# Optimization experiments

Measured on AMD Instinct MI355X. Metric: run time of the kernel, lower is better.

## Reference

```python
import jax, jax.numpy as jnp
import numpy as np

K = 8          # filter_volume = 2^3
N_IN = 1600000 # active input sites
R = 200000     # rules per filter offset (each input site used once total)
N_OUT = 400000 # active output sites
C_IN = 32
C_OUT = 32


def setup_inputs() -> dict:
    key = jax.random.key(0)
    k1, k2, k3, k4 = jax.random.split(key, 4)
    std = (2.0 * 1 / C_IN / K) ** 0.5  # SCN init: sqrt(2*groups/nIn/filter_volume)
    input_features = jax.random.normal(k1, (N_IN, C_IN), dtype=jnp.float32)
    weight = jax.random.normal(k2, (K, 1, C_IN, C_OUT), dtype=jnp.float32) * std
    bias = jnp.zeros((C_OUT,), dtype=jnp.float32)
    # Rulebook: per filter offset f, pairs (rules_in[f,r] -> rules_out[f,r]).
    # For a 2^3/stride-2 conv each input site appears exactly once overall;
    # a random permutation split into K chunks models that structure.
    perm = jax.random.permutation(k3, N_IN)[: K * R]
    rules_in = perm.reshape(K, R).astype(jnp.int32)
    rules_out = jax.random.randint(k4, (K, R), 0, N_OUT, dtype=jnp.int32)
    return {
        "input_features": input_features,
        "weight": weight,
        "bias": bias,
        "rules_in": rules_in,
        "rules_out": rules_out,
        "n_out": N_OUT,
    }


def reference(input_features, weight, bias, rules_in, rules_out, n_out):
    # gather -> per-offset GEMM -> scatter-add (groups == 1)
    gathered = input_features[rules_in]                 # [K, R, C_in]
    w = weight[:, 0]                                    # [K, C_in, C_out]
    contrib = jnp.einsum("krc,kco->kro", gathered, w)   # [K, R, C_out]
    out = jnp.zeros((n_out, contrib.shape[-1]), dtype=input_features.dtype)
    out = out.at[rules_out.reshape(-1)].add(contrib.reshape(-1, contrib.shape[-1]))
    return out + bias
```

## Files before the change

### kernel.cpp

```cpp
#include <hip/hip_runtime.h>
#include <stdint.h>

#define KTAPS 8
#define C 32
#define CAPR 16
#define OMAX 8192

__global__ __launch_bounds__(256) void init_kernel(
    unsigned int* __restrict__ counts, int n_cnt4) {
  int i = blockIdx.x * 256 + threadIdx.x;
  if (i < n_cnt4) ((uint4*)counts)[i] = make_uint4(0u, 0u, 0u, 0u);
}

__global__ __launch_bounds__(256) void contrib_kernel(
    const float* __restrict__ in, const float* __restrict__ w,
    const int* __restrict__ rules_in, const int* __restrict__ rules_out,
    unsigned int* __restrict__ counts, unsigned int* __restrict__ bidx,
    uint2* __restrict__ oflow, unsigned int* __restrict__ ocount,
    float* __restrict__ contrib, int R) {
  const int k = blockIdx.y;
  const int r = blockIdx.x * 256 + threadIdx.x;
  if (r >= R) return;

  const int ri = rules_in[k * R + r];
  const int ro = rules_out[k * R + r];

  const float4* rowp = (const float4*)(in + (size_t)ri * C);
  float4 av[8];
#pragma unroll
  for (int j = 0; j < 8; ++j) av[j] = rowp[j];

  const unsigned int slot = atomicAdd(counts + (unsigned int)ro, 1u);

  float a[C];
#pragma unroll
  for (int j = 0; j < 8; ++j) {
    a[4 * j + 0] = av[j].x; a[4 * j + 1] = av[j].y;
    a[4 * j + 2] = av[j].z; a[4 * j + 3] = av[j].w;
  }

  const float* wk = w + k * (C * C);
  float acc[C];
#pragma unroll
  for (int co = 0; co < C; ++co) acc[co] = a[0] * wk[co];
#pragma unroll
  for (int ci = 1; ci < C; ++ci)
#pragma unroll
    for (int co = 0; co < C; ++co)
      acc[co] = fmaf(a[ci], wk[ci * C + co], acc[co]);

  const unsigned int t = (unsigned int)(k * R + r);
  float4* cp = (float4*)(contrib + (size_t)t * C);
#pragma unroll
  for (int j = 0; j < 8; ++j)
    cp[j] = make_float4(acc[4 * j + 0], acc[4 * j + 1],
                        acc[4 * j + 2], acc[4 * j + 3]);

  if (slot < (unsigned int)CAPR) {
    bidx[(size_t)(unsigned int)ro * CAPR + slot] = t;
  } else {
    unsigned int j = atomicAdd(ocount, 1u);
    if (j < (unsigned int)OMAX) oflow[j] = make_uint2((unsigned int)ro, t);
  }
}

__global__ __launch_bounds__(256) void reduce_kernel(
    const unsigned int* __restrict__ counts,
    const unsigned int* __restrict__ bidx,
    const float* __restrict__ contrib, const float* __restrict__ bias,
    float* __restrict__ out, int n_out) {
  const int g    = threadIdx.x >> 5;
  const int lane = threadIdx.x & 31;
  const int rowA = (blockIdx.x * 8 + g) * 2;
  if (rowA >= n_out) return;
  const int rowB = rowA + 1;

  const unsigned int bval = bidx[(size_t)rowA * CAPR + lane];
  unsigned int cntA = counts[rowA]; if (cntA > (unsigned int)CAPR) cntA = CAPR;
  unsigned int cntB = counts[rowB]; if (cntB > (unsigned int)CAPR) cntB = CAPR;

  float vA[CAPR], vB[CAPR];
#pragma unroll
  for (int j = 0; j < CAPR; ++j) {
    const unsigned int tA = (unsigned int)__shfl((int)bval, j, 32);
    const unsigned int sA = (j < (int)cntA) ? tA : 0u;
    vA[j] = contrib[(size_t)sA * C + lane];
  }
#pragma unroll
  for (int j = 0; j < CAPR; ++j) {
    const unsigned int tB = (unsigned int)__shfl((int)bval, CAPR + j, 32);
    const unsigned int sB = (j < (int)cntB) ? tB : 0u;
    vB[j] = contrib[(size_t)sB * C + lane];
  }

  const float b = bias[lane];
  float accA = b, accB = b;
#pragma unroll
  for (int j = 0; j < CAPR; ++j) {
    accA += (j < (int)cntA) ? vA[j] : 0.f;
    accB += (j < (int)cntB) ? vB[j] : 0.f;
  }

  out[(size_t)rowA * C + lane] = accA;
  out[(size_t)rowB * C + lane] = accB;
}

__global__ __launch_bounds__(256) void oflow_kernel(
    const uint2* __restrict__ oflow, const unsigned int* __restrict__ ocount,
    const float* __restrict__ contrib, float* __restrict__ out) {
  const int g  = threadIdx.x >> 5;
  const int co = threadIdx.x & 31;
  unsigned int n = *ocount;
  if (n > (unsigned int)OMAX) n = (unsigned int)OMAX;
  for (unsigned int e = blockIdx.x * 8 + g; e < n; e += gridDim.x * 8) {
    const uint2 ent = oflow[e];
    unsafeAtomicAdd(out + (size_t)ent.x * C + co,
                    contrib[(size_t)ent.y * C + co]);
  }
}

__global__ __launch_bounds__(256) void bias_init_kernel(
    float* __restrict__ out, const float* __restrict__ bias, int n4) {
  int idx = blockIdx.x * 256 + threadIdx.x;
  if (idx >= n4) return;
  ((float4*)out)[idx] = ((const float4*)bias)[idx & 7];
}

__global__ __launch_bounds__(256) void scatter_gemm_kernel(
    const float* __restrict__ in, const float* __restrict__ w,
    const int* __restrict__ rules_in, const int* __restrict__ rules_out,
    float* __restrict__ out, int R) {
  const int k = blockIdx.y;
  const int r = blockIdx.x * 256 + threadIdx.x;
  if (r >= R) return;
  const int ri = rules_in[k * R + r];
  const int ro = rules_out[k * R + r];
  const float4* rowp = (const float4*)(in + (size_t)ri * C);
  float a[C];
#pragma unroll
  for (int j = 0; j < 8; ++j) {
    float4 vv = rowp[j];
    a[4 * j + 0] = vv.x; a[4 * j + 1] = vv.y;
    a[4 * j + 2] = vv.z; a[4 * j + 3] = vv.w;
  }
  const float* wk = w + k * (C * C);
  float acc[C];
#pragma unroll
  for (int co = 0; co < C; ++co) acc[co] = a[0] * wk[co];
#pragma unroll
  for (int ci = 1; ci < C; ++ci)
#pragma unroll
    for (int co = 0; co < C; ++co)
      acc[co] = fmaf(a[ci], wk[ci * C + co], acc[co]);
  float* op = out + (size_t)ro * C;
#pragma unroll
  for (int co = 0; co < C; ++co) unsafeAtomicAdd(op + co, acc[co]);
}

extern "C" void kernel_launch(void* const* d_in, const int* in_sizes, int n_in,
                              void* d_out, int out_size, void* d_ws, size_t ws_size,
                              hipStream_t stream) {
  const float* in_features = (const float*)d_in[0];
  const float* weight      = (const float*)d_in[1];
  const float* bias        = (const float*)d_in[2];
  const int*   rules_in    = (const int*)d_in[3];
  const int*   rules_out   = (const int*)d_in[4];

  const int R     = in_sizes[3] / KTAPS;
  const int n_out = out_size / C;
  float* out = (float*)d_out;

  const size_t n_cnt     = ((size_t)n_out + 16) & ~(size_t)3;
  const size_t counts_b  = n_cnt * sizeof(unsigned int);
  const size_t bidx_b    = (size_t)n_out * CAPR * sizeof(unsigned int);
  const size_t oflow_b   = (size_t)OMAX * sizeof(uint2);
  const size_t n_rules   = (size_t)KTAPS * R;
  const size_t contrib_b = n_rules * C * sizeof(float);

  if (ws_size >= counts_b + bidx_b + oflow_b + contrib_b) {
    unsigned int* counts  = (unsigned int*)d_ws;
    unsigned int* ocount  = counts + n_out;
    unsigned int* bidx    = (unsigned int*)((char*)d_ws + counts_b);
    uint2*        oflow   = (uint2*)((char*)d_ws + counts_b + bidx_b);
    float*        contrib = (float*)((char*)d_ws + counts_b + bidx_b + oflow_b);

    const int n_cnt4 = (int)(n_cnt / 4);
    init_kernel<<<(n_cnt4 + 255) / 256, 256, 0, stream>>>(counts, n_cnt4);

    dim3 gridB((R + 255) / 256, KTAPS);
    contrib_kernel<<<gridB, 256, 0, stream>>>(in_features, weight, rules_in,
                                              rules_out, counts, bidx, oflow,
                                              ocount, contrib, R);

    const int rows_per_block = 16;
    reduce_kernel<<<(n_out + rows_per_block - 1) / rows_per_block, 256, 0,
                    stream>>>(counts, bidx, contrib, bias, out, n_out);

    oflow_kernel<<<32, 256, 0, stream>>>(oflow, ocount, contrib, out);
  } else {
    const int n_out4 = out_size / 4;
    bias_init_kernel<<<(n_out4 + 255) / 256, 256, 0, stream>>>(out, bias, n_out4);
    dim3 grid((R + 255) / 256, KTAPS);
    scatter_gemm_kernel<<<grid, 256, 0, stream>>>(in_features, weight, rules_in,
                                                  rules_out, out, R);
  }
}
```

Measured before the change: 471.3 us.

## Fuse GEMM and scatter with LDS-transposed coalesced atomics, drop bucketed reduction

Replaces the contribution-buffer plus bucketed-reduction pipeline with a single kernel that computes each rule's 32-wide GEMM row, stages it in padded shared memory, and issues row-coalesced float atomics directly into the bias-initialised output. This removes the large intermediate contrib write/read and the count/index bookkeeping. In exchange it relies on atomic throughput to random output rows and gives up deterministic summation order.

```diff
diff --git a/kernel.cpp b/kernel.cpp
--- a/kernel.cpp
+++ b/kernel.cpp
@@ -3,34 +3,40 @@
 
 #define KTAPS 8
 #define C 32
-#define CAPR 16
-#define OMAX 8192
+#define LDSS 33
 
-__global__ __launch_bounds__(256) void init_kernel(
-    unsigned int* __restrict__ counts, int n_cnt4) {
-  int i = blockIdx.x * 256 + threadIdx.x;
-  if (i < n_cnt4) ((uint4*)counts)[i] = make_uint4(0u, 0u, 0u, 0u);
+__global__ __launch_bounds__(256) void bias_init_kernel(
+    float* __restrict__ out, const float* __restrict__ bias, int n4) {
+  int idx = blockIdx.x * 256 + threadIdx.x;
+  if (idx >= n4) return;
+  ((float4*)out)[idx] = ((const float4*)bias)[idx & 7];
 }
 
-__global__ __launch_bounds__(256) void contrib_kernel(
+__global__ __launch_bounds__(256) void fused_scatter_kernel(
     const float* __restrict__ in, const float* __restrict__ w,
     const int* __restrict__ rules_in, const int* __restrict__ rules_out,
-    unsigned int* __restrict__ counts, unsigned int* __restrict__ bidx,
-    uint2* __restrict__ oflow, unsigned int* __restrict__ ocount,
-    float* __restrict__ contrib, int R) {
-  const int k = blockIdx.y;
-  const int r = blockIdx.x * 256 + threadIdx.x;
-  if (r >= R) return;
+    float* __restrict__ out, int R) {
+  __shared__ float cbuf[256 * LDSS];
+  __shared__ int   robuf[256];
 
-  const int ri = rules_in[k * R + r];
-  const int ro = rules_out[k * R + r];
+  const int k     = blockIdx.y;
+  const int tid   = threadIdx.x;
+  const int r     = blockIdx.x * 256 + tid;
+  const int lane  = tid & 63;
+  const int wbase = tid & ~63;
+
+  if (blockIdx.x * 256 + wbase >= R) return;
+
+  const bool valid = (r < R);
+  const int rc = valid ? r : (R - 1);
+  const int ri = rules_in[(size_t)k * R + rc];
+  const int ro = valid ? rules_out[(size_t)k * R + rc] : -1;
+  robuf[tid] = ro;
 
   const float4* rowp = (const float4*)(in + (size_t)ri * C);
   float4 av[8];
 #pragma unroll
   for (int j = 0; j < 8; ++j) av[j] = rowp[j];
-
-  const unsigned int slot = atomicAdd(counts + (unsigned int)ro, 1u);
 
   float a[C];
 #pragma unroll
@@ -49,112 +55,20 @@
     for (int co = 0; co < C; ++co)
       acc[co] = fmaf(a[ci], wk[ci * C + co], acc[co]);
 
-  const unsigned int t = (unsigned int)(k * R + r);
-  float4* cp = (float4*)(contrib + (size_t)t * C);
+  float* myrow = cbuf + tid * LDSS;
 #pragma unroll
-  for (int j = 0; j < 8; ++j)
-    cp[j] = make_float4(acc[4 * j + 0], acc[4 * j + 1],
-                        acc[4 * j + 2], acc[4 * j + 3]);
+  for (int co = 0; co < C; ++co) myrow[co] = acc[co];
 
-  if (slot < (unsigned int)CAPR) {
-    bidx[(size_t)(unsigned int)ro * CAPR + slot] = t;
-  } else {
-    unsigned int j = atomicAdd(ocount, 1u);
-    if (j < (unsigned int)OMAX) oflow[j] = make_uint2((unsigned int)ro, t);
+  const int co   = lane & 31;
+  const int half = lane >> 5;
+#pragma unroll
+  for (int j = 0; j < 32; ++j) {
+    const int rl  = wbase + 2 * j + half;
+    const int rol = robuf[rl];
+    const float v = cbuf[rl * LDSS + co];
+    if (rol >= 0)
+      unsafeAtomicAdd(out + (size_t)rol * C + co, v);
   }
-}
-
-__global__ __launch_bounds__(256) void reduce_kernel(
-    const unsigned int* __restrict__ counts,
-    const unsigned int* __restrict__ bidx,
-    const float* __restrict__ contrib, const float* __restrict__ bias,
-    float* __restrict__ out, int n_out) {
-  const int g    = threadIdx.x >> 5;
-  const int lane = threadIdx.x & 31;
-  const int rowA = (blockIdx.x * 8 + g) * 2;
-  if (rowA >= n_out) return;
-  const int rowB = rowA + 1;
-
-  const unsigned int bval = bidx[(size_t)rowA * CAPR + lane];
-  unsigned int cntA = counts[rowA]; if (cntA > (unsigned int)CAPR) cntA = CAPR;
-  unsigned int cntB = counts[rowB]; if (cntB > (unsigned int)CAPR) cntB = CAPR;
-
-  float vA[CAPR], vB[CAPR];
-#pragma unroll
-  for (int j = 0; j < CAPR; ++j) {
-    const unsigned int tA = (unsigned int)__shfl((int)bval, j, 32);
-    const unsigned int sA = (j < (int)cntA) ? tA : 0u;
-    vA[j] = contrib[(size_t)sA * C + lane];
-  }
-#pragma unroll
-  for (int j = 0; j < CAPR; ++j) {
-    const unsigned int tB = (unsigned int)__shfl((int)bval, CAPR + j, 32);
-    const unsigned int sB = (j < (int)cntB) ? tB : 0u;
-    vB[j] = contrib[(size_t)sB * C + lane];
-  }
-
-  const float b = bias[lane];
-  float accA = b, accB = b;
-#pragma unroll
-  for (int j = 0; j < CAPR; ++j) {
-    accA += (j < (int)cntA) ? vA[j] : 0.f;
-    accB += (j < (int)cntB) ? vB[j] : 0.f;
-  }
-
-  out[(size_t)rowA * C + lane] = accA;
-  out[(size_t)rowB * C + lane] = accB;
-}
-
-__global__ __launch_bounds__(256) void oflow_kernel(
-    const uint2* __restrict__ oflow, const unsigned int* __restrict__ ocount,
-    const float* __restrict__ contrib, float* __restrict__ out) {
-  const int g  = threadIdx.x >> 5;
-  const int co = threadIdx.x & 31;
-  unsigned int n = *ocount;
-  if (n > (unsigned int)OMAX) n = (unsigned int)OMAX;
-  for (unsigned int e = blockIdx.x * 8 + g; e < n; e += gridDim.x * 8) {
-    const uint2 ent = oflow[e];
-    unsafeAtomicAdd(out + (size_t)ent.x * C + co,
-                    contrib[(size_t)ent.y * C + co]);
-  }
-}
-
-__global__ __launch_bounds__(256) void bias_init_kernel(
-    float* __restrict__ out, const float* __restrict__ bias, int n4) {
-  int idx = blockIdx.x * 256 + threadIdx.x;
-  if (idx >= n4) return;
-  ((float4*)out)[idx] = ((const float4*)bias)[idx & 7];
-}
-
-__global__ __launch_bounds__(256) void scatter_gemm_kernel(
-    const float* __restrict__ in, const float* __restrict__ w,
-    const int* __restrict__ rules_in, const int* __restrict__ rules_out,
-    float* __restrict__ out, int R) {
-  const int k = blockIdx.y;
-  const int r = blockIdx.x * 256 + threadIdx.x;
-  if (r >= R) return;
-  const int ri = rules_in[k * R + r];
-  const int ro = rules_out[k * R + r];
-  const float4* rowp = (const float4*)(in + (size_t)ri * C);
-  float a[C];
-#pragma unroll
-  for (int j = 0; j < 8; ++j) {
-    float4 vv = rowp[j];
-    a[4 * j + 0] = vv.x; a[4 * j + 1] = vv.y;
-    a[4 * j + 2] = vv.z; a[4 * j + 3] = vv.w;
-  }
-  const float* wk = w + k * (C * C);
-  float acc[C];
-#pragma unroll
-  for (int co = 0; co < C; ++co) acc[co] = a[0] * wk[co];
-#pragma unroll
-  for (int ci = 1; ci < C; ++ci)
-#pragma unroll
-    for (int co = 0; co < C; ++co)
-      acc[co] = fmaf(a[ci], wk[ci * C + co], acc[co]);
-  float* op = out + (size_t)ro * C;
-#pragma unroll
-  for (int co = 0; co < C; ++co) unsafeAtomicAdd(op + co, acc[co]);
 }
 
 extern "C" void kernel_launch(void* const* d_in, const int* in_sizes, int n_in,
@@ -166,42 +80,13 @@
   const int*   rules_in    = (const int*)d_in[3];
   const int*   rules_out   = (const int*)d_in[4];
 
-  const int R     = in_sizes[3] / KTAPS;
-  const int n_out = out_size / C;
+  const int R = in_sizes[3] / KTAPS;
   float* out = (float*)d_out;
 
-  const size_t n_cnt     = ((size_t)n_out + 16) & ~(size_t)3;
-  const size_t counts_b  = n_cnt * sizeof(unsigned int);
-  const size_t bidx_b    = (size_t)n_out * CAPR * sizeof(unsigned int);
-  const size_t oflow_b   = (size_t)OMAX * sizeof(uint2);
-  const size_t n_rules   = (size_t)KTAPS * R;
-  const size_t contrib_b = n_rules * C * sizeof(float);
+  const int n_out4 = out_size / 4;
+  bias_init_kernel<<<(n_out4 + 255) / 256, 256, 0, stream>>>(out, bias, n_out4);
 
-  if (ws_size >= counts_b + bidx_b + oflow_b + contrib_b) {
-    unsigned int* counts  = (unsigned int*)d_ws;
-    unsigned int* ocount  = counts + n_out;
-    unsigned int* bidx    = (unsigned int*)((char*)d_ws + counts_b);
-    uint2*        oflow   = (uint2*)((char*)d_ws + counts_b + bidx_b);
-    float*        contrib = (float*)((char*)d_ws + counts_b + bidx_b + oflow_b);
-
-    const int n_cnt4 = (int)(n_cnt / 4);
-    init_kernel<<<(n_cnt4 + 255) / 256, 256, 0, stream>>>(counts, n_cnt4);
-
-    dim3 gridB((R + 255) / 256, KTAPS);
-    contrib_kernel<<<gridB, 256, 0, stream>>>(in_features, weight, rules_in,
-                                              rules_out, counts, bidx, oflow,
-                                              ocount, contrib, R);
-
-    const int rows_per_block = 16;
-    reduce_kernel<<<(n_out + rows_per_block - 1) / rows_per_block, 256, 0,
-                    stream>>>(counts, bidx, contrib, bias, out, n_out);
-
-    oflow_kernel<<<32, 256, 0, stream>>>(oflow, ocount, contrib, out);
-  } else {
-    const int n_out4 = out_size / 4;
-    bias_init_kernel<<<(n_out4 + 255) / 256, 256, 0, stream>>>(out, bias, n_out4);
-    dim3 grid((R + 255) / 256, KTAPS);
-    scatter_gemm_kernel<<<grid, 256, 0, stream>>>(in_features, weight, rules_in,
-                                                  rules_out, out, R);
-  }
+  dim3 grid((R + 255) / 256, KTAPS);
+  fused_scatter_kernel<<<grid, 256, 0, stream>>>(in_features, weight, rules_in,
+                                                 rules_out, out, R);
 }
```

Measured after the change: 407.1 us. 13.6% less time.
